# Kernel tuning notes

Measured on AMD Instinct MI355X. Metric: run time of the kernel, lower is better.

Reference implementation:

```python
import jax, jax.numpy as jnp
import numpy as np

B, S, D_MODEL, N_HEADS = 2, 2048, 1024, 16
HEAD_DIM = D_MODEL // N_HEADS  # 64
SCALE = HEAD_DIM ** -0.5
MASK_FILL = -1e9


def setup_inputs() -> dict:
    key = jax.random.key(0)
    k1, k2, k3 = jax.random.split(key, 3)
    x = jax.random.normal(k1, (B, S, D_MODEL), dtype=jnp.float32)
    # nn.Linear weight [3*d_att, d_model], trunc_normal std=0.02 style init
    W_qkv = jax.random.normal(k2, (3 * D_MODEL, D_MODEL), dtype=jnp.float32) * 0.02
    # boolean attention mask over the full [b, s_q, h, t_k] score tensor (True = keep)
    mask = jax.random.bernoulli(k3, p=0.9, shape=(B, S, N_HEADS, S))
    return {"x": x, "W_qkv": W_qkv, "mask": mask}


def reference(x, W_qkv, mask):
    b, s, dm = x.shape
    h, d = N_HEADS, HEAD_DIM
    # fused QKV projection (no bias): [b,s,3*dm] -> [b,s,3,h,d]
    qkv = jnp.einsum('bsm,nm->bsn', x, W_qkv).reshape(b, s, 3, h, d)
    q, k, v = qkv[:, :, 0], qkv[:, :, 1], qkv[:, :, 2]
    # scores: [b, s_q, h, t_k]
    attn = jnp.einsum('bshd,bthd->bsht', q, k) * SCALE
    attn = jnp.where(mask, attn, MASK_FILL)
    attn = jax.nn.softmax(attn, axis=-1)
    # out[b,t,h,d] = sum_s attn[b,t,h,s] * v[b,s,h,d]  (original einsum 'b s h d, b t h s -> b t h d')
    out = jnp.einsum('bshd,bths->bthd', v, attn)
    return out.reshape(b, s, h * d)  # proj is Identity (d_out=None)
```

## Files before the change

kernel.cpp:

```cpp
#include <hip/hip_runtime.h>

#define S_   2048
#define DM_  1024
#define NH_  16
#define HD_  64
#define KDIM 1024

typedef __attribute__((ext_vector_type(8))) short  shortx8;
typedef __attribute__((ext_vector_type(4))) float  floatx4;

#define AS1 __attribute__((address_space(1)))
#define AS3 __attribute__((address_space(3)))

__device__ __forceinline__ unsigned short f2bf(float f) {
  unsigned u = __float_as_uint(f);
  u += 0x7FFFu + ((u >> 16) & 1u);
  return (unsigned short)(u >> 16);
}

__device__ __forceinline__ void gld_lds16(const void* g, unsigned short* l) {
  __builtin_amdgcn_global_load_lds((const AS1 void*)g, (AS3 void*)l, 16, 0, 0);
}

__global__ __launch_bounds__(256) void detect_kernel(const unsigned* __restrict__ mask,
                                                     const unsigned* __restrict__ x,
                                                     int* __restrict__ flags)
{
  __shared__ int s[5];
  if (threadIdx.x == 0) { s[0]=1; s[1]=1; s[2]=1; s[3]=1; s[4]=0; }
  __syncthreads();
  bool o32=true, of32=true, o16=true, o8=true;
  for (int i = threadIdx.x; i < 16384; i += 256) {
    unsigned v = mask[i];
    o32 &= (v <= 1u);
    of32 &= (v == 0u) || (v == 0x3F800000u);
    unsigned lo = v & 0xFFFFu, hi = v >> 16;
    o16 &= ((lo==0u)||(lo==0x3F80u)) && ((hi==0u)||(hi==0x3F80u));
    o8  &= ((v & 0xFEFEFEFEu) == 0u);
  }
  int cnt = 0;
  for (int i = threadIdx.x; i < 4096; i += 256) {
    unsigned v = x[i];
    unsigned b1 = (v >> 8) & 0x7Fu;
    cnt += (b1 >= 0x32u && b1 <= 0x41u) ? 1 : 0;
  }
  if (!o32)  atomicAnd(&s[0], 0);
  if (!of32) atomicAnd(&s[1], 0);
  if (!o16)  atomicAnd(&s[2], 0);
  if (!o8)   atomicAnd(&s[3], 0);
  atomicAdd(&s[4], cnt);
  __syncthreads();
  if (threadIdx.x == 0) {
    int mf;
    if (s[0]) mf = 0; else if (s[1]) mf = 3; else if (s[2]) mf = 2; else mf = 1;
    flags[0] = mf;
    flags[1] = (s[4] > 2048) ? 1 : 0;
  }
}

__global__ __launch_bounds__(256) void qkv_gemm(const void* __restrict__ Xv,
                                                const void* __restrict__ Wv,
                                                unsigned short* __restrict__ Qg,
                                                unsigned short* __restrict__ Kg,
                                                unsigned short* __restrict__ Vt,
                                                const int* __restrict__ flags)
{
  __shared__ unsigned short lA[128*64];
  __shared__ unsigned short lB[128*64];
  const int tid  = threadIdx.x;
  const int wid  = tid >> 6,  lane = tid & 63;
  const int quad = lane >> 4, l16  = lane & 15;
  const int bm = blockIdx.x, bn = blockIdx.y;
  const int wM = (wid >> 1) * 64, wN = (wid & 1) * 64;
  const int xbf = flags[1];

  floatx4 acc[4][4] = {};

  for (int kt = 0; kt < KDIM; kt += 64) {
    __syncthreads();
    if (xbf) {
      const unsigned short* X = (const unsigned short*)Xv;
      const unsigned short* W = (const unsigned short*)Wv;
      #pragma unroll
      for (int p = 0; p < 4; ++p) {
        int chunk = p*256 + tid;
        int r = chunk >> 3, c = chunk & 7;
        gld_lds16(X + (size_t)(bm*128 + r)*KDIM + kt + c*8, lA + chunk*8);
      }
      #pragma unroll
      for (int p = 0; p < 4; ++p) {
        int chunk = p*256 + tid;
        int r = chunk >> 3, c = chunk & 7;
        gld_lds16(W + (size_t)(bn*128 + r)*KDIM + kt + c*8, lB + chunk*8);
      }
    } else {
      const float* X = (const float*)Xv;
      const float* W = (const float*)Wv;
      #pragma unroll
      for (int p = 0; p < 8; ++p) {
        int c4 = p*256 + tid;
        int r = c4 >> 4, c = c4 & 15;
        float4 v = *(const float4*)(X + (size_t)(bm*128 + r)*KDIM + kt + c*4);
        unsigned short* d = lA + r*64 + c*4;
        d[0]=f2bf(v.x); d[1]=f2bf(v.y); d[2]=f2bf(v.z); d[3]=f2bf(v.w);
      }
      #pragma unroll
      for (int p = 0; p < 8; ++p) {
        int c4 = p*256 + tid;
        int r = c4 >> 4, c = c4 & 15;
        float4 v = *(const float4*)(W + (size_t)(bn*128 + r)*KDIM + kt + c*4);
        unsigned short* d = lB + r*64 + c*4;
        d[0]=f2bf(v.x); d[1]=f2bf(v.y); d[2]=f2bf(v.z); d[3]=f2bf(v.w);
      }
    }
    __syncthreads();

    #pragma unroll
    for (int ks = 0; ks < 2; ++ks) {
      shortx8 af[4], bfr[4];
      #pragma unroll
      for (int mi = 0; mi < 4; ++mi)
        af[mi] = *(const shortx8*)(lA + (wM + mi*16 + l16)*64 + ks*32 + quad*8);
      #pragma unroll
      for (int ni = 0; ni < 4; ++ni)
        bfr[ni] = *(const shortx8*)(lB + (wN + ni*16 + l16)*64 + ks*32 + quad*8);
      #pragma unroll
      for (int mi = 0; mi < 4; ++mi)
        #pragma unroll
        for (int ni = 0; ni < 4; ++ni)
          acc[mi][ni] = __builtin_amdgcn_mfma_f32_16x16x32_bf16(af[mi], bfr[ni], acc[mi][ni], 0, 0, 0);
    }
  }

  if (bn < 8) {
    #pragma unroll
    for (int mi = 0; mi < 4; ++mi)
      #pragma unroll
      for (int ni = 0; ni < 4; ++ni)
        #pragma unroll
        for (int r = 0; r < 4; ++r) {
          int m = bm*128 + wM + mi*16 + quad*4 + r;
          int n = bn*128 + wN + ni*16 + l16;
          int b = m >> 11, q = m & 2047, h = n >> 6, d = n & 63;
          Qg[(((size_t)(b*NH_ + h))*S_ + q)*HD_ + d] = f2bf(acc[mi][ni][r] * 0.125f);
        }
  } else if (bn < 16) {
    #pragma unroll
    for (int mi = 0; mi < 4; ++mi)
      #pragma unroll
      for (int ni = 0; ni < 4; ++ni)
        #pragma unroll
        for (int r = 0; r < 4; ++r) {
          int m = bm*128 + wM + mi*16 + quad*4 + r;
          int n = bn*128 + wN + ni*16 + l16 - 1024;
          int b = m >> 11, t = m & 2047, h = n >> 6, d = n & 63;
          Kg[(((size_t)(b*NH_ + h))*S_ + t)*HD_ + d] = f2bf(acc[mi][ni][r]);
        }
  } else {
    #pragma unroll
    for (int mi = 0; mi < 4; ++mi)
      #pragma unroll
      for (int ni = 0; ni < 4; ++ni) {
        int m0 = bm*128 + wM + mi*16 + quad*4;
        int n  = bn*128 + wN + ni*16 + l16 - 2048;
        int b = m0 >> 11, t = m0 & 2047, h = n >> 6, d = n & 63;
        ushort4 u;
        u.x = f2bf(acc[mi][ni][0]); u.y = f2bf(acc[mi][ni][1]);
        u.z = f2bf(acc[mi][ni][2]); u.w = f2bf(acc[mi][ni][3]);
        *(ushort4*)(Vt + (((size_t)(b*NH_ + h))*HD_ + d)*S_ + t) = u;
      }
  }
}

__global__ __launch_bounds__(256) void attn_kernel(const unsigned short* __restrict__ Qg,
                                                   const unsigned short* __restrict__ Kg,
                                                   const unsigned short* __restrict__ Vt,
                                                   const void* __restrict__ maskp,
                                                   const int* __restrict__ flags,
                                                   void* __restrict__ outv)
{
  __shared__ unsigned short lQ[64*64];
  __shared__ unsigned short lK[64*64];
  __shared__ unsigned short lVt[64*64];
  __shared__ unsigned short lP[4][16*72];

  const int tid  = threadIdx.x;
  const int wid  = tid >> 6,  lane = tid & 63;
  const int quad = lane >> 4, l16  = lane & 15;
  const int qb = blockIdx.x * 64;
  const int h  = blockIdx.y, b = blockIdx.z;
  const int bh = b*NH_ + h;
  const int mflag = flags[0];
  const int obf   = flags[1];

  #pragma unroll
  for (int p = 0; p < 2; ++p) {
    int chunk = p*256 + tid;
    gld_lds16(Qg + ((size_t)bh*S_ + qb)*HD_ + chunk*8, lQ + chunk*8);
  }
  __syncthreads();

  shortx8 qf[2];
  #pragma unroll
  for (int ks = 0; ks < 2; ++ks)
    qf[ks] = *(const shortx8*)(lQ + (wid*16 + l16)*64 + ks*32 + quad*8);

  floatx4 acc[4] = {};
  float lsum[4] = {0.f, 0.f, 0.f, 0.f};

  size_t mbase[4];
  #pragma unroll
  for (int r = 0; r < 4; ++r) {
    int q = qb + wid*16 + quad*4 + r;
    mbase[r] = (((size_t)b*S_ + q)*NH_ + h)*S_ + l16;
  }

  for (int t0 = 0; t0 < S_; t0 += 64) {
    __syncthreads();
    #pragma unroll
    for (int p = 0; p < 2; ++p) {
      int chunk = p*256 + tid;
      gld_lds16(Kg + ((size_t)bh*S_ + t0)*HD_ + chunk*8, lK + chunk*8);
    }
    #pragma unroll
    for (int p = 0; p < 2; ++p) {
      int chunk = p*256 + tid;
      int r = chunk >> 3, c = chunk & 7;
      gld_lds16(Vt + ((size_t)bh*HD_ + r)*S_ + t0 + c*8, lVt + chunk*8);
    }

    unsigned mnz[4][4];
    if (mflag == 0) {
      const unsigned* mp = (const unsigned*)maskp;
      #pragma unroll
      for (int tile = 0; tile < 4; ++tile)
        #pragma unroll
        for (int r = 0; r < 4; ++r) mnz[tile][r] = mp[mbase[r] + t0 + tile*16];
    } else if (mflag == 1) {
      const unsigned char* mp = (const unsigned char*)maskp;
      #pragma unroll
      for (int tile = 0; tile < 4; ++tile)
        #pragma unroll
        for (int r = 0; r < 4; ++r) mnz[tile][r] = mp[mbase[r] + t0 + tile*16];
    } else if (mflag == 2) {
      const unsigned short* mp = (const unsigned short*)maskp;
      #pragma unroll
      for (int tile = 0; tile < 4; ++tile)
        #pragma unroll
        for (int r = 0; r < 4; ++r) mnz[tile][r] = mp[mbase[r] + t0 + tile*16];
    } else {
      const unsigned* mp = (const unsigned*)maskp;
      #pragma unroll
      for (int tile = 0; tile < 4; ++tile)
        #pragma unroll
        for (int r = 0; r < 4; ++r) mnz[tile][r] = mp[mbase[r] + t0 + tile*16];
    }
    __syncthreads();

    floatx4 sc[4] = {};
    #pragma unroll
    for (int tile = 0; tile < 4; ++tile)
      #pragma unroll
      for (int ks = 0; ks < 2; ++ks) {
        shortx8 kf = *(const shortx8*)(lK + (tile*16 + l16)*64 + ks*32 + quad*8);
        sc[tile] = __builtin_amdgcn_mfma_f32_16x16x32_bf16(qf[ks], kf, sc[tile], 0, 0, 0);
      }

    float pv[4][4];
    #pragma unroll
    for (int tile = 0; tile < 4; ++tile)
      #pragma unroll
      for (int r = 0; r < 4; ++r) {
        float e = __expf(sc[tile][r]);
        pv[tile][r] = mnz[tile][r] ? e : 0.f;
        lsum[r] += pv[tile][r];
      }

    unsigned short* lPw = lP[wid];
    #pragma unroll
    for (int tile = 0; tile < 4; ++tile)
      #pragma unroll
      for (int r = 0; r < 4; ++r)
        lPw[(quad*4 + r)*72 + tile*16 + l16] = f2bf(pv[tile][r]);

    #pragma unroll
    for (int ks = 0; ks < 2; ++ks) {
      shortx8 pa = *(const shortx8*)(lPw + l16*72 + ks*32 + quad*8);
      #pragma unroll
      for (int d = 0; d < 4; ++d) {
        shortx8 vb = *(const shortx8*)(lVt + (d*16 + l16)*64 + ks*32 + quad*8);
        acc[d] = __builtin_amdgcn_mfma_f32_16x16x32_bf16(pa, vb, acc[d], 0, 0, 0);
      }
    }
  }

  float rinv[4];
  #pragma unroll
  for (int r = 0; r < 4; ++r) {
    float l = lsum[r];
    #pragma unroll
    for (int o = 1; o < 16; o <<= 1) l += __shfl_xor(l, o);
    rinv[r] = 1.f / l;
  }

  #pragma unroll
  for (int d = 0; d < 4; ++d)
    #pragma unroll
    for (int r = 0; r < 4; ++r) {
      int q = qb + wid*16 + quad*4 + r;
      size_t oi = ((size_t)b*S_ + q)*DM_ + h*HD_ + d*16 + l16;
      float v = acc[d][r] * rinv[r];
      if (obf) ((unsigned short*)outv)[oi] = f2bf(v);
      else     ((float*)outv)[oi]          = v;
    }
}

extern "C" void kernel_launch(void* const* d_in, const int* in_sizes, int n_in,
                              void* d_out, int out_size, void* d_ws, size_t ws_size,
                              hipStream_t stream) {
  (void)in_sizes; (void)n_in; (void)out_size; (void)ws_size;
  const void* X    = d_in[0];
  const void* W    = d_in[1];
  const void* mask = d_in[2];
  int* flags = (int*)d_ws;
  const size_t SEG = (size_t)2*NH_*S_*HD_*2;
  unsigned short* Qg = (unsigned short*)((char*)d_ws + 256);
  unsigned short* Kg = (unsigned short*)((char*)d_ws + 256 + SEG);
  unsigned short* Vt = (unsigned short*)((char*)d_ws + 256 + 2*SEG);

  detect_kernel<<<1, 256, 0, stream>>>((const unsigned*)mask, (const unsigned*)X, flags);
  qkv_gemm<<<dim3(32, 24), 256, 0, stream>>>(X, W, Qg, Kg, Vt, flags);
  attn_kernel<<<dim3(32, 16, 2), 256, 0, stream>>>(Qg, Kg, Vt, mask, flags, d_out);
}
```

Measured before the change: 882.2 us.

## Double-buffer K/V tiles and prefetch mask in attention loop

The attention loop now keeps two LDS buffers for K and V^T and issues the next tile's global-to-LDS loads and mask loads before computing on the current tile. This overlaps memory latency with MFMA work and needs one barrier per iteration instead of two. The Q staging area is reused as the per-wave P scratch with an XOR swizzle in place of padding, so LDS use stays bounded and bank conflicts are meant to drop. Launch bounds now request four blocks per CU. The prefetched mask is held in extra registers, which raises register pressure.

```diff
diff --git a/kernel.cpp b/kernel.cpp
--- a/kernel.cpp
+++ b/kernel.cpp
@@ -172,17 +172,16 @@
   }
 }
 
-__global__ __launch_bounds__(256) void attn_kernel(const unsigned short* __restrict__ Qg,
-                                                   const unsigned short* __restrict__ Kg,
-                                                   const unsigned short* __restrict__ Vt,
-                                                   const void* __restrict__ maskp,
-                                                   const int* __restrict__ flags,
-                                                   void* __restrict__ outv)
+__global__ __launch_bounds__(256, 4) void attn_kernel(const unsigned short* __restrict__ Qg,
+                                                      const unsigned short* __restrict__ Kg,
+                                                      const unsigned short* __restrict__ Vt,
+                                                      const void* __restrict__ maskp,
+                                                      const int* __restrict__ flags,
+                                                      void* __restrict__ outv)
 {
-  __shared__ unsigned short lQ[64*64];
-  __shared__ unsigned short lK[64*64];
-  __shared__ unsigned short lVt[64*64];
-  __shared__ unsigned short lP[4][16*72];
+  __shared__ unsigned short lK[2][64*64];
+  __shared__ unsigned short lVt[2][64*64];
+  __shared__ unsigned short lQP[4][16*64];
 
   const int tid  = threadIdx.x;
   const int wid  = tid >> 6,  lane = tid & 63;
@@ -196,102 +195,110 @@
   #pragma unroll
   for (int p = 0; p < 2; ++p) {
     int chunk = p*256 + tid;
-    gld_lds16(Qg + ((size_t)bh*S_ + qb)*HD_ + chunk*8, lQ + chunk*8);
-  }
-  __syncthreads();
-
-  shortx8 qf[2];
-  #pragma unroll
-  for (int ks = 0; ks < 2; ++ks)
-    qf[ks] = *(const shortx8*)(lQ + (wid*16 + l16)*64 + ks*32 + quad*8);
-
-  floatx4 acc[4] = {};
-  float lsum[4] = {0.f, 0.f, 0.f, 0.f};
-
-  size_t mbase[4];
-  #pragma unroll
-  for (int r = 0; r < 4; ++r) {
-    int q = qb + wid*16 + quad*4 + r;
-    mbase[r] = (((size_t)b*S_ + q)*NH_ + h)*S_ + l16;
-  }
-
-  for (int t0 = 0; t0 < S_; t0 += 64) {
-    __syncthreads();
+    gld_lds16(Qg + ((size_t)bh*S_ + qb)*HD_ + chunk*8, (unsigned short*)lQP + chunk*8);
+  }
+
+  auto stage = [&](int t0, int buf) {
     #pragma unroll
     for (int p = 0; p < 2; ++p) {
       int chunk = p*256 + tid;
-      gld_lds16(Kg + ((size_t)bh*S_ + t0)*HD_ + chunk*8, lK + chunk*8);
+      gld_lds16(Kg + ((size_t)bh*S_ + t0)*HD_ + chunk*8, lK[buf] + chunk*8);
     }
     #pragma unroll
     for (int p = 0; p < 2; ++p) {
       int chunk = p*256 + tid;
       int r = chunk >> 3, c = chunk & 7;
-      gld_lds16(Vt + ((size_t)bh*HD_ + r)*S_ + t0 + c*8, lVt + chunk*8);
-    }
-
-    unsigned mnz[4][4];
-    if (mflag == 0) {
-      const unsigned* mp = (const unsigned*)maskp;
+      gld_lds16(Vt + ((size_t)bh*HD_ + r)*S_ + t0 + c*8, lVt[buf] + chunk*8);
+    }
+  };
+
+  size_t mrow[4];
+  #pragma unroll
+  for (int r = 0; r < 4; ++r) {
+    int q = qb + wid*16 + quad*4 + r;
+    mrow[r] = (((size_t)b*S_ + q)*NH_ + h)*S_ + l16;
+  }
+
+  auto loadmask = [&](int t0, unsigned (*mz)[4]) {
+    if (mflag == 1) {
+      const unsigned char* mp = (const unsigned char*)maskp;
       #pragma unroll
       for (int tile = 0; tile < 4; ++tile)
         #pragma unroll
-        for (int r = 0; r < 4; ++r) mnz[tile][r] = mp[mbase[r] + t0 + tile*16];
-    } else if (mflag == 1) {
-      const unsigned char* mp = (const unsigned char*)maskp;
-      #pragma unroll
-      for (int tile = 0; tile < 4; ++tile)
-        #pragma unroll
-        for (int r = 0; r < 4; ++r) mnz[tile][r] = mp[mbase[r] + t0 + tile*16];
+        for (int r = 0; r < 4; ++r) mz[tile][r] = mp[mrow[r] + t0 + tile*16];
     } else if (mflag == 2) {
       const unsigned short* mp = (const unsigned short*)maskp;
       #pragma unroll
       for (int tile = 0; tile < 4; ++tile)
         #pragma unroll
-        for (int r = 0; r < 4; ++r) mnz[tile][r] = mp[mbase[r] + t0 + tile*16];
+        for (int r = 0; r < 4; ++r) mz[tile][r] = mp[mrow[r] + t0 + tile*16];
     } else {
       const unsigned* mp = (const unsigned*)maskp;
       #pragma unroll
       for (int tile = 0; tile < 4; ++tile)
         #pragma unroll
-        for (int r = 0; r < 4; ++r) mnz[tile][r] = mp[mbase[r] + t0 + tile*16];
-    }
-    __syncthreads();
+        for (int r = 0; r < 4; ++r) mz[tile][r] = mp[mrow[r] + t0 + tile*16];
+    }
+  };
+
+  unsigned mc[4][4], mn[4][4];
+  stage(0, 0);
+  loadmask(0, mc);
+  __syncthreads();
+
+  shortx8 qf[2];
+  #pragma unroll
+  for (int ks = 0; ks < 2; ++ks)
+    qf[ks] = *(const shortx8*)((const unsigned short*)lQP + (wid*16 + l16)*64 + ks*32 + quad*8);
+
+  floatx4 acc[4] = {};
+  float lsum[4] = {0.f, 0.f, 0.f, 0.f};
+  unsigned short* lPw = lQP[wid];
+
+  for (int t0 = 0; t0 < S_; t0 += 64) {
+    const int cur = (t0 >> 6) & 1;
+    if (t0 + 64 < S_) {
+      stage(t0 + 64, cur ^ 1);
+      loadmask(t0 + 64, mn);
+    }
 
     floatx4 sc[4] = {};
     #pragma unroll
     for (int tile = 0; tile < 4; ++tile)
       #pragma unroll
       for (int ks = 0; ks < 2; ++ks) {
-        shortx8 kf = *(const shortx8*)(lK + (tile*16 + l16)*64 + ks*32 + quad*8);
+        shortx8 kf = *(const shortx8*)(lK[cur] + (tile*16 + l16)*64 + ks*32 + quad*8);
         sc[tile] = __builtin_amdgcn_mfma_f32_16x16x32_bf16(qf[ks], kf, sc[tile], 0, 0, 0);
       }
 
-    float pv[4][4];
     #pragma unroll
     for (int tile = 0; tile < 4; ++tile)
       #pragma unroll
       for (int r = 0; r < 4; ++r) {
         float e = __expf(sc[tile][r]);
-        pv[tile][r] = mnz[tile][r] ? e : 0.f;
-        lsum[r] += pv[tile][r];
-      }
-
-    unsigned short* lPw = lP[wid];
+        e = mc[tile][r] ? e : 0.f;
+        lsum[r] += e;
+        int row = quad*4 + r;
+        int col = tile*16 + l16;
+        lPw[(row << 6) + (((col >> 3) ^ (row & 7)) << 3) + (col & 7)] = f2bf(e);
+      }
+
+    #pragma unroll
+    for (int ks = 0; ks < 2; ++ks) {
+      shortx8 pa = *(const shortx8*)(lPw + (l16 << 6) + ((((ks*4 + quad)) ^ (l16 & 7)) << 3));
+      #pragma unroll
+      for (int d = 0; d < 4; ++d) {
+        shortx8 vb = *(const shortx8*)(lVt[cur] + (d*16 + l16)*64 + ks*32 + quad*8);
+        acc[d] = __builtin_amdgcn_mfma_f32_16x16x32_bf16(pa, vb, acc[d], 0, 0, 0);
+      }
+    }
+
     #pragma unroll
     for (int tile = 0; tile < 4; ++tile)
       #pragma unroll
-      for (int r = 0; r < 4; ++r)
-        lPw[(quad*4 + r)*72 + tile*16 + l16] = f2bf(pv[tile][r]);
-
-    #pragma unroll
-    for (int ks = 0; ks < 2; ++ks) {
-      shortx8 pa = *(const shortx8*)(lPw + l16*72 + ks*32 + quad*8);
-      #pragma unroll
-      for (int d = 0; d < 4; ++d) {
-        shortx8 vb = *(const shortx8*)(lVt + (d*16 + l16)*64 + ks*32 + quad*8);
-        acc[d] = __builtin_amdgcn_mfma_f32_16x16x32_bf16(pa, vb, acc[d], 0, 0, 0);
-      }
-    }
+      for (int r = 0; r < 4; ++r) mc[tile][r] = mn[tile][r];
+
+    __syncthreads();
   }
 
   float rinv[4];
```

After: 886.4 us. No clear change (+0.5%).
